# Kernel optimization log

Measured on AMD Instinct MI355X. Metric: run time of the kernel, lower is better.

The kernel has to match this reference:

```python
import jax, jax.numpy as jnp
import numpy as np

HEADS = 16
LOCAL_ATTN_CTX = 128  # band half-width for attn_mode='local'
NEG = -1e9


def setup_inputs() -> dict:
    key = jax.random.key(0)
    kq, kk, kv = jax.random.split(key, 3)
    B, N, D = 1, 2048, 1024
    q = jax.random.normal(kq, (B, N, D), dtype=jnp.float32)
    k = jax.random.normal(kk, (B, N, D), dtype=jnp.float32)
    v = jax.random.normal(kv, (B, N, D), dtype=jnp.float32)
    return {"q": q, "k": k, "v": v}


def _split_heads(x, h):
    # [B, N, D] -> [B, H, N, Dh]
    B, N, D = x.shape
    return x.reshape(B, N, h, D // h).transpose(0, 2, 1, 3)


def _local_mask(n, ctx):
    # band mask: 1 where |i-j| <= ctx, matching sum of diag ones in torch code
    idx = jnp.arange(n)
    return (jnp.abs(idx[:, None] - idx[None, :]) <= ctx).astype(jnp.float32)


def reference(q, k, v):
    B, N, D = q.shape
    qh = _split_heads(q, HEADS)  # [B,H,N,Dh]
    kh = _split_heads(k, HEADS)
    vh = _split_heads(v, HEADS)
    dh = D // HEADS
    scale = 1.0 / np.sqrt(dh).astype(np.float32)
    mask = _local_mask(N, LOCAL_ATTN_CTX)  # [N,N]
    w = jnp.einsum('bhnd,bhmd->bhnm', qh, kh) * scale
    w = w * mask + NEG * (1.0 - mask)
    w = jax.nn.softmax(w, axis=-1)
    a = jnp.einsum('bhnm,bhmd->bhnd', w, vh)  # [B,H,N,Dh]
    # merge heads: [B,H,N,Dh] -> [B,N,D]
    return a.transpose(0, 2, 1, 3).reshape(B, N, D)
```

## Files before the change

### kernel.cpp

```cpp
#include <hip/hip_runtime.h>
#include <math.h>

#define HEADS 16
#define SEQ_N 2048
#define DMODEL 1024
#define DH 64
#define CTX 128
#define QBLK 64
#define KBLK 32
#define LDK 72
#define LDV 36
#define KELEM (KBLK * LDK)
#define VELEM (DH * LDV)

typedef __attribute__((ext_vector_type(8))) short short8;
typedef __attribute__((ext_vector_type(4))) float f32x4;

__device__ __forceinline__ ushort f2bf(float f) {
    union { float f; unsigned u; } a; a.f = f;
    return (ushort)((a.u + 0x7FFFu + ((a.u >> 16) & 1u)) >> 16);
}
__device__ __forceinline__ short8 pack8(float4 a, float4 b) {
    short8 s;
    s[0] = (short)f2bf(a.x); s[1] = (short)f2bf(a.y);
    s[2] = (short)f2bf(a.z); s[3] = (short)f2bf(a.w);
    s[4] = (short)f2bf(b.x); s[5] = (short)f2bf(b.y);
    s[6] = (short)f2bf(b.z); s[7] = (short)f2bf(b.w);
    return s;
}
__device__ __forceinline__ short8 mk_frag(const ushort* p0, const ushort* p1) {
    union { unsigned long long u[2]; short8 s; } cv;
    cv.u[0] = *(const unsigned long long*)p0;
    cv.u[1] = *(const unsigned long long*)p1;
    return cv.s;
}

__global__ __launch_bounds__(256) void sattn_mfma2(
    const float* __restrict__ qg, const float* __restrict__ kg,
    const float* __restrict__ vg, float* __restrict__ out)
{
    __shared__ ushort kt[2][2][KELEM];
    __shared__ ushort vt[2][2][VELEM];

    const int h     = blockIdx.x;
    const int qbase = blockIdx.y * QBLK;
    const int t     = threadIdx.x;
    const int wave  = t >> 6;
    const int lane  = t & 63;
    const int lq    = lane & 15;
    const int g     = lane >> 4;

    const int iq = qbase + wave * 16 + lq;

    const int jlo  = max(0, qbase - CTX);
    const int jhi  = min(SEQ_N - 1, qbase + QBLK - 1 + CTX);
    const int nch  = (jhi - jlo + 1) / KBLK;
    const int nchH = nch >> 1;
    const int jbase0 = jlo;
    const int jbase1 = jlo + nchH * KBLK;

    const float qs = 0.18033688011112042f;
    short8 qf[2];
    {
        const float* qrow = qg + (size_t)iq * DMODEL + h * DH;
        #pragma unroll
        for (int kc = 0; kc < 2; ++kc) {
            float4 f0 = *(const float4*)(qrow + kc * 32 + g * 4);
            float4 f1 = *(const float4*)(qrow + kc * 32 + 16 + g * 4);
            f0.x *= qs; f0.y *= qs; f0.z *= qs; f0.w *= qs;
            f1.x *= qs; f1.y *= qs; f1.z *= qs; f1.w *= qs;
            qf[kc] = pack8(f0, f1);
        }
    }

    f32x4 oacc[4];
    #pragma unroll
    for (int dt = 0; dt < 4; ++dt) oacc[dt] = (f32x4){0.f, 0.f, 0.f, 0.f};
    float lsum = 0.f;

    const int srow = t >> 3;
    const int sdg  = t & 7;

    float4 pk[2][2], pv[2][2];
    auto prefetch = [&](int it2) {
        #pragma unroll
        for (int hf = 0; hf < 2; ++hf) {
            const int j = ((hf == 0) ? jbase0 : jbase1) + it2 * KBLK + srow;
            const float* kp = kg + (size_t)j * DMODEL + h * DH + sdg * 8;
            const float* vp = vg + (size_t)j * DMODEL + h * DH + sdg * 8;
            pk[hf][0] = ((const float4*)kp)[0]; pk[hf][1] = ((const float4*)kp)[1];
            pv[hf][0] = ((const float4*)vp)[0]; pv[hf][1] = ((const float4*)vp)[1];
        }
    };
    auto stage = [&](int buf) {
        #pragma unroll
        for (int hf = 0; hf < 2; ++hf) {
            *(short8*)&kt[buf][hf][srow * LDK + sdg * 8] = pack8(pk[hf][0], pk[hf][1]);
            short8 vb = pack8(pv[hf][0], pv[hf][1]);
            #pragma unroll
            for (int e = 0; e < 8; ++e)
                vt[buf][hf][(sdg * 8 + e) * LDV + srow] = (ushort)vb[e];
        }
    };

    prefetch(0);
    stage(0);
    __syncthreads();

    for (int it = 0; it < nchH; ++it) {
        const int cur = it & 1;
        const bool more = (it + 1 < nchH);
        if (more) prefetch(it + 1);

        f32x4 st[2][2];
        #pragma unroll
        for (int hf = 0; hf < 2; ++hf) {
            st[hf][0] = (f32x4){0.f, 0.f, 0.f, 0.f};
            st[hf][1] = (f32x4){0.f, 0.f, 0.f, 0.f};
            #pragma unroll
            for (int kc = 0; kc < 2; ++kc) {
                const ushort* kr0 = &kt[cur][hf][lq * LDK + kc * 32 + g * 4];
                const ushort* kr1 = &kt[cur][hf][(16 + lq) * LDK + kc * 32 + g * 4];
                st[hf][0] = __builtin_amdgcn_mfma_f32_16x16x32_bf16(
                    mk_frag(kr0, kr0 + 16), qf[kc], st[hf][0], 0, 0, 0);
                st[hf][1] = __builtin_amdgcn_mfma_f32_16x16x32_bf16(
                    mk_frag(kr1, kr1 + 16), qf[kc], st[hf][1], 0, 0, 0);
            }
        }

        short8 pf[2];
        #pragma unroll
        for (int hf = 0; hf < 2; ++hf) {
            const int jc    = ((hf == 0) ? jbase0 : jbase1) + it * KBLK;
            const int dbase = jc - iq + CTX;
            float psum = 0.f;
            #pragma unroll
            for (int r = 0; r < 4; ++r) {
                const int loc0 = g * 4 + r;
                const float s0 = ((unsigned)(dbase + loc0)      <= 2u * CTX) ? st[hf][0][r] : -1.0e30f;
                const float s1 = ((unsigned)(dbase + loc0 + 16) <= 2u * CTX) ? st[hf][1][r] : -1.0e30f;
                const float p0 = exp2f(s0);
                const float p1 = exp2f(s1);
                psum += p0 + p1;
                pf[hf][r]     = (short)f2bf(p0);
                pf[hf][4 + r] = (short)f2bf(p1);
            }
            lsum += psum;
        }

        #pragma unroll
        for (int dt = 0; dt < 4; ++dt) {
            #pragma unroll
            for (int hf = 0; hf < 2; ++hf) {
                const ushort* vr = &vt[cur][hf][(dt * 16 + lq) * LDV + g * 4];
                oacc[dt] = __builtin_amdgcn_mfma_f32_16x16x32_bf16(
                    mk_frag(vr, vr + 16), pf[hf], oacc[dt], 0, 0, 0);
            }
        }

        if (more) stage(cur ^ 1);
        __syncthreads();
    }

    lsum += __shfl_xor(lsum, 16);
    lsum += __shfl_xor(lsum, 32);
    const float inv = 1.0f / lsum;
    float* orow = out + (size_t)iq * DMODEL + h * DH;
    #pragma unroll
    for (int dt = 0; dt < 4; ++dt) {
        float4 o;
        o.x = oacc[dt][0] * inv; o.y = oacc[dt][1] * inv;
        o.z = oacc[dt][2] * inv; o.w = oacc[dt][3] * inv;
        *(float4*)&orow[dt * 16 + g * 4] = o;
    }
}

extern "C" void kernel_launch(void* const* d_in, const int* in_sizes, int n_in,
                              void* d_out, int out_size, void* d_ws, size_t ws_size,
                              hipStream_t stream) {
    const float* q = (const float*)d_in[0];
    const float* k = (const float*)d_in[1];
    const float* v = (const float*)d_in[2];
    float* out = (float*)d_out;

    dim3 grid(HEADS, SEQ_N / QBLK);
    dim3 block(256);
    sattn_mfma2<<<grid, block, 0, stream>>>(q, k, v, out);
}
```

Measured before the change: 18.10 us.

## Split key range across wave pairs with 32-query blocks and LDS merge

Each block now handles 32 queries instead of 64. Its four waves form two pairs, and each pair covers one half of the key band, so the grid grows to 1024 blocks and each wave does half the MFMA work per chunk. The partial outputs and row sums from the second half are combined through a shared-memory buffer that reuses the K/V tile storage via a union. The change also adds a launch-bounds occupancy hint, a block-index swizzle over query windows, and s_setprio around the compute. Per-query K/V reuse drops, so each block reloads a relatively larger band, and an extra barrier plus merge step are added.

```diff
diff --git a/kernel.cpp b/kernel.cpp
--- a/kernel.cpp
+++ b/kernel.cpp
@@ -6,12 +6,13 @@
 #define DMODEL 1024
 #define DH 64
 #define CTX 128
-#define QBLK 64
+#define QW 32
 #define KBLK 32
 #define LDK 72
 #define LDV 36
 #define KELEM (KBLK * LDK)
 #define VELEM (DH * LDV)
+#define MSTR 17
 
 typedef __attribute__((ext_vector_type(8))) short short8;
 typedef __attribute__((ext_vector_type(4))) float f32x4;
@@ -35,34 +36,42 @@
     return cv.s;
 }
 
-__global__ __launch_bounds__(256) void sattn_mfma2(
-    const float* __restrict__ qg, const float* __restrict__ kg,
-    const float* __restrict__ vg, float* __restrict__ out)
+__global__ __launch_bounds__(256, 4) void sattn_split2(
+    const float* __restrict__ qm, const float* __restrict__ km,
+    const float* __restrict__ vm, float* __restrict__ out)
 {
-    __shared__ ushort kt[2][2][KELEM];
-    __shared__ ushort vt[2][2][VELEM];
-
-    const int h     = blockIdx.x;
-    const int qbase = blockIdx.y * QBLK;
-    const int t     = threadIdx.x;
-    const int wave  = t >> 6;
-    const int lane  = t & 63;
-    const int lq    = lane & 15;
-    const int g     = lane >> 4;
-
-    const int iq = qbase + wave * 16 + lq;
+    union Smem {
+        struct { ushort kt[2][2][KELEM]; ushort vt[2][2][VELEM]; } tl;
+        float mbuf[2][64][MSTR];
+    };
+    __shared__ Smem sm;
+
+    const int b = blockIdx.x;
+    const int w = (b & 7) * 8 + ((b >> 3) & 7);
+    const int h = b >> 6;
+
+    const int qbase = w * QW;
+    const int t    = threadIdx.x;
+    const int wave = t >> 6;
+    const int lane = t & 63;
+    const int half = wave & 1;
+    const int qgi  = wave >> 1;
+    const int lq   = lane & 15;
+    const int g    = lane >> 4;
+    const int iq   = qbase + qgi * 16 + lq;
 
     const int jlo  = max(0, qbase - CTX);
-    const int jhi  = min(SEQ_N - 1, qbase + QBLK - 1 + CTX);
-    const int nch  = (jhi - jlo + 1) / KBLK;
-    const int nchH = nch >> 1;
-    const int jbase0 = jlo;
-    const int jbase1 = jlo + nchH * KBLK;
+    const int jhi  = min(SEQ_N - 1, qbase + QW - 1 + CTX);
+    const int nch  = (jhi - jlo + 1) >> 5;
+    const int nchA = (nch + 1) >> 1;
+    const int nchB = nch >> 1;
+    const int myn  = half ? nchB : nchA;
+    const int jmyb = jlo + (half ? nchA * KBLK : 0);
 
     const float qs = 0.18033688011112042f;
     short8 qf[2];
     {
-        const float* qrow = qg + (size_t)iq * DMODEL + h * DH;
+        const float* qrow = qm + (size_t)iq * DMODEL + h * DH;
         #pragma unroll
         for (int kc = 0; kc < 2; ++kc) {
             float4 f0 = *(const float4*)(qrow + kc * 32 + g * 4);
@@ -80,14 +89,16 @@
 
     const int srow = t >> 3;
     const int sdg  = t & 7;
+    const int jbs[2]  = { jlo, jlo + nchA * KBLK };
+    const int lims[2] = { nchA, nchB };
 
     float4 pk[2][2], pv[2][2];
-    auto prefetch = [&](int it2) {
+    auto prefetch = [&](int it) {
         #pragma unroll
         for (int hf = 0; hf < 2; ++hf) {
-            const int j = ((hf == 0) ? jbase0 : jbase1) + it2 * KBLK + srow;
-            const float* kp = kg + (size_t)j * DMODEL + h * DH + sdg * 8;
-            const float* vp = vg + (size_t)j * DMODEL + h * DH + sdg * 8;
+            const int j = (it < lims[hf]) ? (jbs[hf] + it * KBLK + srow) : (jlo + srow);
+            const float* kp = km + (size_t)j * DMODEL + h * DH + sdg * 8;
+            const float* vp = vm + (size_t)j * DMODEL + h * DH + sdg * 8;
             pk[hf][0] = ((const float4*)kp)[0]; pk[hf][1] = ((const float4*)kp)[1];
             pv[hf][0] = ((const float4*)vp)[0]; pv[hf][1] = ((const float4*)vp)[1];
         }
@@ -95,11 +106,11 @@
     auto stage = [&](int buf) {
         #pragma unroll
         for (int hf = 0; hf < 2; ++hf) {
-            *(short8*)&kt[buf][hf][srow * LDK + sdg * 8] = pack8(pk[hf][0], pk[hf][1]);
+            *(short8*)&sm.tl.kt[buf][hf][srow * LDK + sdg * 8] = pack8(pk[hf][0], pk[hf][1]);
             short8 vb = pack8(pv[hf][0], pv[hf][1]);
             #pragma unroll
             for (int e = 0; e < 8; ++e)
-                vt[buf][hf][(sdg * 8 + e) * LDV + srow] = (ushort)vb[e];
+                sm.tl.vt[buf][hf][(sdg * 8 + e) * LDV + srow] = (ushort)vb[e];
         }
     };
 
@@ -107,55 +118,49 @@
     stage(0);
     __syncthreads();
 
-    for (int it = 0; it < nchH; ++it) {
+    for (int it = 0; it < nchA; ++it) {
         const int cur = it & 1;
-        const bool more = (it + 1 < nchH);
+        const bool more = (it + 1 < nchA);
         if (more) prefetch(it + 1);
 
-        f32x4 st[2][2];
-        #pragma unroll
-        for (int hf = 0; hf < 2; ++hf) {
-            st[hf][0] = (f32x4){0.f, 0.f, 0.f, 0.f};
-            st[hf][1] = (f32x4){0.f, 0.f, 0.f, 0.f};
+        if (it < myn) {
+            __builtin_amdgcn_s_setprio(1);
+            f32x4 st0 = (f32x4){0.f, 0.f, 0.f, 0.f};
+            f32x4 st1 = (f32x4){0.f, 0.f, 0.f, 0.f};
             #pragma unroll
             for (int kc = 0; kc < 2; ++kc) {
-                const ushort* kr0 = &kt[cur][hf][lq * LDK + kc * 32 + g * 4];
-                const ushort* kr1 = &kt[cur][hf][(16 + lq) * LDK + kc * 32 + g * 4];
-                st[hf][0] = __builtin_amdgcn_mfma_f32_16x16x32_bf16(
-                    mk_frag(kr0, kr0 + 16), qf[kc], st[hf][0], 0, 0, 0);
-                st[hf][1] = __builtin_amdgcn_mfma_f32_16x16x32_bf16(
-                    mk_frag(kr1, kr1 + 16), qf[kc], st[hf][1], 0, 0, 0);
+                const ushort* kr0 = &sm.tl.kt[cur][half][lq * LDK + kc * 32 + g * 4];
+                const ushort* kr1 = &sm.tl.kt[cur][half][(16 + lq) * LDK + kc * 32 + g * 4];
+                st0 = __builtin_amdgcn_mfma_f32_16x16x32_bf16(
+                    mk_frag(kr0, kr0 + 16), qf[kc], st0, 0, 0, 0);
+                st1 = __builtin_amdgcn_mfma_f32_16x16x32_bf16(
+                    mk_frag(kr1, kr1 + 16), qf[kc], st1, 0, 0, 0);
             }
-        }
-
-        short8 pf[2];
-        #pragma unroll
-        for (int hf = 0; hf < 2; ++hf) {
-            const int jc    = ((hf == 0) ? jbase0 : jbase1) + it * KBLK;
+
+            const int jc    = jmyb + it * KBLK;
             const int dbase = jc - iq + CTX;
+            short8 pf;
             float psum = 0.f;
             #pragma unroll
             for (int r = 0; r < 4; ++r) {
                 const int loc0 = g * 4 + r;
-                const float s0 = ((unsigned)(dbase + loc0)      <= 2u * CTX) ? st[hf][0][r] : -1.0e30f;
-                const float s1 = ((unsigned)(dbase + loc0 + 16) <= 2u * CTX) ? st[hf][1][r] : -1.0e30f;
+                const float s0 = ((unsigned)(dbase + loc0)      <= 2u * CTX) ? st0[r] : -1.0e30f;
+                const float s1 = ((unsigned)(dbase + loc0 + 16) <= 2u * CTX) ? st1[r] : -1.0e30f;
                 const float p0 = exp2f(s0);
                 const float p1 = exp2f(s1);
                 psum += p0 + p1;
-                pf[hf][r]     = (short)f2bf(p0);
-                pf[hf][4 + r] = (short)f2bf(p1);
+                pf[r]     = (short)f2bf(p0);
+                pf[4 + r] = (short)f2bf(p1);
             }
             lsum += psum;
-        }
-
-        #pragma unroll
-        for (int dt = 0; dt < 4; ++dt) {
-            #pragma unroll
-            for (int hf = 0; hf < 2; ++hf) {
-                const ushort* vr = &vt[cur][hf][(dt * 16 + lq) * LDV + g * 4];
+
+            #pragma unroll
+            for (int dt = 0; dt < 4; ++dt) {
+                const ushort* vr = &sm.tl.vt[cur][half][(dt * 16 + lq) * LDV + g * 4];
                 oacc[dt] = __builtin_amdgcn_mfma_f32_16x16x32_bf16(
-                    mk_frag(vr, vr + 16), pf[hf], oacc[dt], 0, 0, 0);
+                    mk_frag(vr, vr + 16), pf, oacc[dt], 0, 0, 0);
             }
+            __builtin_amdgcn_s_setprio(0);
         }
 
         if (more) stage(cur ^ 1);
@@ -164,14 +169,33 @@
 
     lsum += __shfl_xor(lsum, 16);
     lsum += __shfl_xor(lsum, 32);
-    const float inv = 1.0f / lsum;
-    float* orow = out + (size_t)iq * DMODEL + h * DH;
-    #pragma unroll
-    for (int dt = 0; dt < 4; ++dt) {
-        float4 o;
-        o.x = oacc[dt][0] * inv; o.y = oacc[dt][1] * inv;
-        o.z = oacc[dt][2] * inv; o.w = oacc[dt][3] * inv;
-        *(float4*)&orow[dt * 16 + g * 4] = o;
+
+    if (half == 1) {
+        float* mb = sm.mbuf[qgi][lane];
+        #pragma unroll
+        for (int dt = 0; dt < 4; ++dt) {
+            #pragma unroll
+            for (int r = 0; r < 4; ++r) mb[dt * 4 + r] = oacc[dt][r];
+        }
+        mb[16] = lsum;
+    }
+    __syncthreads();
+    if (half == 0) {
+        const float* mb = sm.mbuf[qgi][lane];
+        #pragma unroll
+        for (int dt = 0; dt < 4; ++dt) {
+            #pragma unroll
+            for (int r = 0; r < 4; ++r) oacc[dt][r] += mb[dt * 4 + r];
+        }
+        const float inv = 1.0f / (lsum + mb[16]);
+        float* orow = out + (size_t)iq * DMODEL + h * DH;
+        #pragma unroll
+        for (int dt = 0; dt < 4; ++dt) {
+            float4 o;
+            o.x = oacc[dt][0] * inv; o.y = oacc[dt][1] * inv;
+            o.z = oacc[dt][2] * inv; o.w = oacc[dt][3] * inv;
+            *(float4*)&orow[dt * 16 + g * 4] = o;
+        }
     }
 }
 
@@ -183,7 +207,7 @@
     const float* v = (const float*)d_in[2];
     float* out = (float*)d_out;
 
-    dim3 grid(HEADS, SEQ_N / QBLK);
+    dim3 grid(HEADS * (SEQ_N / QW));
     dim3 block(256);
-    sattn_mfma2<<<grid, block, 0, stream>>>(q, k, v, out);
-}
+    sattn_split2<<<grid, block, 0, stream>>>(q, k, v, out);
+}
```

New measurement: 22.06 us. +21.9%, slower.
